# Performance work log

Hardware: AMD Instinct MI355X
Metric: run time of the kernel (lower is better)

The kernel has to match this reference:

```python
import jax, jax.numpy as jnp
import numpy as np

B, IN, HID = 8192, 2048, 2048


def setup_inputs() -> dict:
    key = jax.random.key(0)
    ks = jax.random.split(key, 8)
    s_in = 1.0 / np.sqrt(IN + HID)  # torch Linear default init scale (uniform bound)
    inp = {
        "x": jax.random.normal(ks[0], (B, IN), jnp.float32),
        "h_prev": jax.random.normal(ks[1], (B, HID), jnp.float32),
        "c_prev": jax.random.normal(ks[2], (B, HID), jnp.float32),
        "embedding_vec": jnp.zeros((B, 1), jnp.float32),  # ignored in vanilla mode
        "Wf": jax.random.normal(ks[3], (IN + HID, HID), jnp.float32) * s_in,
        "Wi": jax.random.normal(ks[4], (IN + HID, HID), jnp.float32) * s_in,
        "Wc": jax.random.normal(ks[5], (IN + HID, HID), jnp.float32) * s_in,
        "Wo": jax.random.normal(ks[6], (IN + HID, HID), jnp.float32) * s_in,
        "bf": jnp.zeros((HID,), jnp.float32),
        "bi": jnp.zeros((HID,), jnp.float32),
        "bc": jnp.zeros((HID,), jnp.float32),
        "bo": jnp.zeros((HID,), jnp.float32),
    }
    return inp


def reference(x, h_prev, c_prev, embedding_vec, Wf, Wi, Wc, Wo, bf, bi, bc, bo):
    # rearrange_inputs: concat flattened x with h_prev; embedding_vec ignored
    cat = jnp.concatenate([x.reshape(x.shape[0], -1), h_prev], axis=1)  # [B, IN+HID]
    # Fuse the four gate GEMMs into one: [B, IN+HID] @ [IN+HID, 4*HID]
    W = jnp.concatenate([Wf, Wi, Wc, Wo], axis=1)
    b = jnp.concatenate([bf, bi, bc, bo], axis=0)
    z = cat @ W + b  # [B, 4*HID]
    zf, zi, zc, zo = jnp.split(z, 4, axis=1)
    f_t = jax.nn.sigmoid(zf)
    i_t = jax.nn.sigmoid(zi)
    c_opt = jnp.tanh(zc)
    c_t = c_prev * f_t + i_t * c_opt
    o_t = jax.nn.sigmoid(zo)
    h_t = o_t * jnp.tanh(c_t)
    return (h_t, c_t)
```

## Files before the change

kernel.cpp:

```cpp
#include <hip/hip_runtime.h>
#include <stdint.h>

#define B_SZ   8192
#define IN_SZ  2048
#define HIDN   2048
#define KTOT   4096
#define BKk    32
#define NKS    (KTOT / BKk)
#define GRID_F 1024

typedef __attribute__((ext_vector_type(8))) short short8;
typedef __attribute__((ext_vector_type(8))) unsigned short ushort8;
typedef __attribute__((ext_vector_type(4))) float float4v;

static __device__ __forceinline__ float bf2f(uint16_t h) {
  union { uint32_t u; float f; } v; v.u = ((uint32_t)h) << 16; return v.f;
}
static __device__ __forceinline__ uint16_t f2bf(float f) {
  union { float f; uint32_t u; } v; v.f = f;
  uint32_t r = v.u + 0x7FFFu + ((v.u >> 16) & 1u);
  return (uint16_t)(r >> 16);
}
static __device__ __forceinline__ float sigmoidf_(float v) {
  return 1.f / (1.f + __expf(-v));
}
static __device__ __forceinline__ float tanhf_(float v) {
  return 1.f - 2.f / (1.f + __expf(2.f * v));
}

static __device__ __forceinline__ ushort8 load8(const void* base, size_t eidx, int isf32) {
  ushort8 r;
  if (isf32) {
    const float* p = (const float*)base + eidx;
    float4v a = *(const float4v*)p;
    float4v b = *(const float4v*)(p + 4);
    r[0] = f2bf(a[0]); r[1] = f2bf(a[1]); r[2] = f2bf(a[2]); r[3] = f2bf(a[3]);
    r[4] = f2bf(b[0]); r[5] = f2bf(b[1]); r[6] = f2bf(b[2]); r[7] = f2bf(b[3]);
  } else {
    r = *(const ushort8*)((const uint16_t*)base + eidx);
  }
  return r;
}

static __device__ __forceinline__ void gll16(const void* g, void* l) {
  __builtin_amdgcn_global_load_lds(
      (const __attribute__((address_space(1))) uint32_t*)g,
      (__attribute__((address_space(3))) uint32_t*)l, 16, 0, 0);
}

static __device__ __forceinline__ void bar() {
  asm volatile("" ::: "memory");
  __builtin_amdgcn_s_barrier();
  asm volatile("" ::: "memory");
}

__global__ __launch_bounds__(64) void detect_kernel(const uint32_t* __restrict__ x,
                                                    int* __restrict__ flag) {
  const int lane = threadIdx.x;
  int cnt = 0;
  #pragma unroll
  for (int s = 0; s < 8; ++s) {
    uint32_t u = x[lane + s * 64];
    int e = (u >> 7) & 0xFF;
    int hit = (e >= 117 && e <= 131) ? 1 : 0;
    cnt += (int)__popcll(__ballot(hit));
  }
  if (lane == 0) *flag = (cnt < 256) ? 1 : 0;
}

__global__ __launch_bounds__(256) void wtrans_kernel(
    const void* __restrict__ Wf, const void* __restrict__ Wi,
    const void* __restrict__ Wc, const void* __restrict__ Wo,
    uint16_t* __restrict__ Wt, const int* __restrict__ flagp)
{
  __shared__ uint16_t tile[64][33];
  const int isf32 = *flagp;
  const int k0 = blockIdx.x * 32;
  const int n0 = blockIdx.y * 64;
  const int g  = blockIdx.z;
  const void* W = (g == 0) ? Wf : (g == 1) ? Wi : (g == 2) ? Wc : Wo;
  const int tid = threadIdx.x;
  {
    const int r  = tid >> 3;
    const int c8 = (tid & 7) * 8;
    ushort8 v = load8(W, (size_t)(k0 + r) * HIDN + n0 + c8, isf32);
    #pragma unroll
    for (int e = 0; e < 8; ++e) tile[c8 + e][r] = v[e];
  }
  __syncthreads();
  {
    const int n  = tid >> 2;
    const int kc = (tid & 3) * 8;
    ushort8 v;
    #pragma unroll
    for (int e = 0; e < 8; ++e) v[e] = tile[n][kc + e];
    *(ushort8*)(Wt + (size_t)((n0 + n) * 4 + g) * KTOT + k0 + kc) = v;
  }
}

__global__ __launch_bounds__(256) void catconv_kernel(
    const void* __restrict__ x, const void* __restrict__ h,
    uint16_t* __restrict__ catB, const int* __restrict__ flagp)
{
  const int isf32 = *flagp;
  const void* src = blockIdx.y ? h : x;
  const size_t t = (size_t)blockIdx.x * 256 + threadIdx.x;
  const int m  = (int)(t >> 8);
  const int k8 = (int)(t & 255) * 8;
  ushort8 v = load8(src, (size_t)m * IN_SZ + k8, isf32);
  *(ushort8*)(catB + (size_t)m * KTOT + (size_t)blockIdx.y * IN_SZ + k8) = v;
}

extern "C" __global__ __launch_bounds__(512, 2) void lstm_fused_kernel(
    const uint16_t* __restrict__ Wt, const uint16_t* __restrict__ catB,
    const void* __restrict__ cprev,
    const void* __restrict__ bfv, const void* __restrict__ biv,
    const void* __restrict__ bcv, const void* __restrict__ bov,
    void* __restrict__ outbase, const int* __restrict__ flagp)
{
  extern __shared__ __align__(16) char ldsbuf[];

  const int isf32 = *flagp;
  const int tid  = threadIdx.x;
  const int lane = tid & 63;
  const int wave = tid >> 6;
  const int l15  = lane & 15;
  const int quad = lane >> 4;
  const int wr   = wave >> 2;
  const int wc   = wave & 3;

  const int bid = blockIdx.x;
  const int xcd = bid & 7, loc = bid >> 3;
  const int nt  = xcd * 4 + (loc & 3);
  const int mt  = loc >> 2;
  const int mB  = mt * 256;
  const int nB  = nt * 256;
  const int nb4 = nt * 64;

  const int srow = lane >> 2;
  const int scol = ((lane & 3) ^ ((lane >> 5) << 1)) * 8;
  const uint16_t* aSrc[2];
  const uint16_t* bSrc[2];
  #pragma unroll
  for (int s = 0; s < 2; ++s) {
    aSrc[s] = Wt   + (size_t)(nB + (s * 8 + wave) * 16 + srow) * KTOT + scol;
    bSrc[s] = catB + (size_t)(mB + (s * 8 + wave) * 16 + srow) * KTOT + scol;
  }

  int offA[8], offB[4];
  #pragma unroll
  for (int i = 0; i < 8; ++i) {
    const int b = (wr * 8 + i) * 1024 + l15 * 64 + quad * 16;
    offA[i] = b ^ (((l15 >> 3) & 1) << 5);
  }
  #pragma unroll
  for (int j = 0; j < 4; ++j) {
    const int b = (wc * 4 + j) * 1024 + l15 * 64 + quad * 16;
    offB[j] = 16384 + (b ^ (((l15 >> 3) & 1) << 5));
  }

  float4v acc[8][4];
  #pragma unroll
  for (int i = 0; i < 8; ++i)
    #pragma unroll
    for (int j = 0; j < 4; ++j)
      acc[i][j] = {0.f, 0.f, 0.f, 0.f};

  #pragma unroll
  for (int tt = 0; tt < 3; ++tt) {
    const size_t kk = (size_t)tt * BKk;
    const int bb = (tt & 3) * 32768 + wave * 1024;
    gll16(aSrc[0] + kk, ldsbuf + bb);
    gll16(aSrc[1] + kk, ldsbuf + bb + 8192);
    gll16(bSrc[0] + kk, ldsbuf + bb + 16384);
    gll16(bSrc[1] + kk, ldsbuf + bb + 16384 + 8192);
  }
  asm volatile("s_waitcnt vmcnt(8)" ::: "memory");
  bar();

#define KSTEP(T, DO_STAGE, VMSTR)                                              \
  {                                                                            \
    const int bb = ((T) & 3) * 32768;                                          \
    short8 af[4], bfr[4];                                                      \
    _Pragma("unroll")                                                          \
    for (int j = 0; j < 4; ++j)                                                \
      bfr[j] = *(const short8*)(ldsbuf + bb + offB[j]);                        \
    _Pragma("unroll")                                                          \
    for (int ii = 0; ii < 4; ++ii)                                             \
      af[ii] = *(const short8*)(ldsbuf + bb + offA[ii]);                       \
    if (DO_STAGE) {                                                            \
      const size_t kk = (size_t)((T) + 3) * BKk;                               \
      const int sb = (((T) + 3) & 3) * 32768 + wave * 1024;                    \
      gll16(aSrc[0] + kk, ldsbuf + sb);                                        \
      gll16(aSrc[1] + kk, ldsbuf + sb + 8192);                                 \
    }                                                                          \
    bar();                                                                     \
    __builtin_amdgcn_s_setprio(1);                                             \
    _Pragma("unroll")                                                          \
    for (int ii = 0; ii < 4; ++ii)                                             \
      _Pragma("unroll")                                                        \
      for (int j = 0; j < 4; ++j)                                              \
        acc[ii][j] = __builtin_amdgcn_mfma_f32_16x16x32_bf16(                  \
            af[ii], bfr[j], acc[ii][j], 0, 0, 0);                              \
    __builtin_amdgcn_s_setprio(0);                                             \
    bar();                                                                     \
    _Pragma("unroll")                                                          \
    for (int ii = 0; ii < 4; ++ii)                                             \
      af[ii] = *(const short8*)(ldsbuf + bb + offA[4 + ii]);                   \
    if (DO_STAGE) {                                                            \
      const size_t kk = (size_t)((T) + 3) * BKk;                               \
      const int sb = (((T) + 3) & 3) * 32768 + 16384 + wave * 1024;            \
      gll16(bSrc[0] + kk, ldsbuf + sb);                                        \
      gll16(bSrc[1] + kk, ldsbuf + sb + 8192);                                 \
    }                                                                          \
    asm volatile("s_waitcnt " VMSTR ::: "memory");                             \
    bar();                                                                     \
    __builtin_amdgcn_s_setprio(1);                                             \
    _Pragma("unroll")                                                          \
    for (int ii = 0; ii < 4; ++ii)                                             \
      _Pragma("unroll")                                                        \
      for (int j = 0; j < 4; ++j)                                              \
        acc[4 + ii][j] = __builtin_amdgcn_mfma_f32_16x16x32_bf16(              \
            af[ii], bfr[j], acc[4 + ii][j], 0, 0, 0);                          \
    __builtin_amdgcn_s_setprio(0);                                             \
    bar();                                                                     \
  }

  for (int t = 0; t < NKS - 3; ++t) KSTEP(t, 1, "vmcnt(8)");
  KSTEP(NKS - 3, 0, "vmcnt(4)");
  KSTEP(NKS - 2, 0, "vmcnt(0)");
  KSTEP(NKS - 1, 0, "vmcnt(0)");
#undef KSTEP

  #pragma unroll
  for (int i = 0; i < 8; ++i) {
    const int ng = nb4 + wr * 32 + i * 4 + quad;
    const float bfx = isf32 ? ((const float*)bfv)[ng] : bf2f(((const uint16_t*)bfv)[ng]);
    const float bix = isf32 ? ((const float*)biv)[ng] : bf2f(((const uint16_t*)biv)[ng]);
    const float bcx = isf32 ? ((const float*)bcv)[ng] : bf2f(((const uint16_t*)bcv)[ng]);
    const float box = isf32 ? ((const float*)bov)[ng] : bf2f(((const uint16_t*)bov)[ng]);
    #pragma unroll
    for (int j = 0; j < 4; ++j) {
      const int mg = mB + wc * 64 + j * 16 + l15;
      float4v z = acc[i][j];
      const float ft  = sigmoidf_(z[0] + bfx);
      const float it  = sigmoidf_(z[1] + bix);
      const float cto = tanhf_(z[2] + bcx);
      const float ot  = sigmoidf_(z[3] + box);
      const float cp  = isf32 ? ((const float*)cprev)[(size_t)mg * HIDN + ng]
                              : bf2f(((const uint16_t*)cprev)[(size_t)mg * HIDN + ng]);
      const float cvv = cp * ft + it * cto;
      acc[i][j][0] = ot * tanhf_(cvv);
      acc[i][j][1] = cvv;
    }
  }

  if (!isf32) {
    uint16_t* hout = (uint16_t*)outbase;
    uint16_t* cout = hout + (size_t)B_SZ * HIDN;
    uint16_t* hb = (uint16_t*)ldsbuf;
    uint16_t* cb = (uint16_t*)(ldsbuf + 32768);
    #pragma unroll
    for (int i = 0; i < 8; ++i) {
      const int ncl = wr * 32 + i * 4 + quad;
      #pragma unroll
      for (int j = 0; j < 4; ++j) {
        const int ml = wc * 64 + j * 16 + l15;
        hb[ml * 64 + ncl] = f2bf(acc[i][j][0]);
        cb[ml * 64 + ncl] = f2bf(acc[i][j][1]);
      }
    }
    bar();
    #pragma unroll
    for (int s = 0; s < 4; ++s) {
      const int off = tid * 16 + s * 8192;
      const int row = off >> 7;
      const int c8  = (off >> 4) & 7;
      const size_t g = (size_t)(mB + row) * HIDN + nb4 + c8 * 8;
      *(ushort8*)(hout + g) = *(const ushort8*)(ldsbuf + off);
      *(ushort8*)(cout + g) = *(const ushort8*)(ldsbuf + 32768 + off);
    }
  } else {
    float* hout = (float*)outbase;
    float* cout = hout + (size_t)B_SZ * HIDN;
    float* fbH = (float*)ldsbuf;
    float* fbC = (float*)(ldsbuf + 65536);
    #pragma unroll
    for (int i = 0; i < 8; ++i) {
      const int ncl = wr * 32 + i * 4 + quad;
      #pragma unroll
      for (int j = 0; j < 4; ++j) {
        const int ml = wc * 64 + j * 16 + l15;
        fbH[ml * 64 + ncl] = acc[i][j][0];
        fbC[ml * 64 + ncl] = acc[i][j][1];
      }
    }
    bar();
    #pragma unroll
    for (int s = 0; s < 8; ++s) {
      const int off = tid * 16 + s * 8192;
      const int row = off >> 8;
      const int c4  = (off >> 4) & 15;
      const size_t g = (size_t)(mB + row) * HIDN + nb4 + c4 * 4;
      *(float4v*)(hout + g) = *(const float4v*)(ldsbuf + off);
      *(float4v*)(cout + g) = *(const float4v*)(ldsbuf + 65536 + off);
    }
  }
}

extern "C" void kernel_launch(void* const* d_in, const int* in_sizes, int n_in,
                              void* d_out, int out_size, void* d_ws, size_t ws_size,
                              hipStream_t stream) {
  const void* x   = d_in[0];
  const void* h   = d_in[1];
  const void* c   = d_in[2];
  const void* Wf  = d_in[4];
  const void* Wi  = d_in[5];
  const void* Wc  = d_in[6];
  const void* Wo  = d_in[7];
  const void* bf_ = d_in[8];
  const void* bi_ = d_in[9];
  const void* bc_ = d_in[10];
  const void* bo_ = d_in[11];

  int*      flag = (int*)d_ws;
  uint16_t* Wt   = (uint16_t*)((char*)d_ws + 256);
  uint16_t* catB = (uint16_t*)((char*)d_ws + 256 + (size_t)64 * 1024 * 1024);

  static int lds_configured = 0;
  if (!lds_configured) {
    hipFuncSetAttribute((const void*)lstm_fused_kernel,
                        hipFuncAttributeMaxDynamicSharedMemorySize, 131072);
    lds_configured = 1;
  }

  hipLaunchKernelGGL(detect_kernel, dim3(1), dim3(64), 0, stream,
                     (const uint32_t*)x, flag);
  hipLaunchKernelGGL(wtrans_kernel, dim3(KTOT / 32, HIDN / 64, 4), dim3(256), 0, stream,
                     Wf, Wi, Wc, Wo, Wt, flag);
  hipLaunchKernelGGL(catconv_kernel, dim3(B_SZ * IN_SZ / (8 * 256), 2, 1), dim3(256), 0, stream,
                     x, h, catB, flag);
  hipLaunchKernelGGL(lstm_fused_kernel, dim3(GRID_F), dim3(512), 131072, stream,
                     Wt, catB, c, bf_, bi_, bc_, bo_, d_out, flag);
}
```

Measured before the change: 889.1 us.

## Widen weight transpose tiles with XOR swizzle and change GEMM LDS swizzle

```diff
diff --git a/kernel.cpp b/kernel.cpp
--- a/kernel.cpp
+++ b/kernel.cpp
@@ -73,28 +73,35 @@
     const void* __restrict__ Wc, const void* __restrict__ Wo,
     uint16_t* __restrict__ Wt, const int* __restrict__ flagp)
 {
-  __shared__ uint16_t tile[64][33];
+  __shared__ uint16_t tile[4 * 64 * 128];
   const int isf32 = *flagp;
-  const int k0 = blockIdx.x * 32;
+  const int k0 = blockIdx.x * 128;
   const int n0 = blockIdx.y * 64;
-  const int g  = blockIdx.z;
-  const void* W = (g == 0) ? Wf : (g == 1) ? Wi : (g == 2) ? Wc : Wo;
   const int tid = threadIdx.x;
-  {
-    const int r  = tid >> 3;
-    const int c8 = (tid & 7) * 8;
-    ushort8 v = load8(W, (size_t)(k0 + r) * HIDN + n0 + c8, isf32);
-    #pragma unroll
-    for (int e = 0; e < 8; ++e) tile[c8 + e][r] = v[e];
+  const void* Wg4[4] = {Wf, Wi, Wc, Wo};
+
+  #pragma unroll
+  for (int s = 0; s < 16; ++s) {
+    const int flat = s * 256 + tid;
+    const int g = flat >> 10;
+    const int r = (flat >> 3) & 127;
+    const int c = flat & 7;
+    ushort8 v = load8(Wg4[g], (size_t)(k0 + r) * HIDN + n0 + c * 8, isf32);
+    uint16_t* trow = tile + (g * 64 + c * 8) * 128 + (r & 7) + 8 * ((r >> 3) ^ c);
+    #pragma unroll
+    for (int e = 0; e < 8; ++e) trow[e * 128] = v[e];
   }
   __syncthreads();
-  {
-    const int n  = tid >> 2;
-    const int kc = (tid & 3) * 8;
-    ushort8 v;
-    #pragma unroll
-    for (int e = 0; e < 8; ++e) v[e] = tile[n][kc + e];
-    *(ushort8*)(Wt + (size_t)((n0 + n) * 4 + g) * KTOT + k0 + kc) = v;
+
+  #pragma unroll
+  for (int s = 0; s < 16; ++s) {
+    const int flat = s * 256 + tid;
+    const int kc = flat & 15;
+    const int np = flat >> 4;
+    const int n  = np >> 2;
+    ushort8 v = *(const ushort8*)(tile + (np & 3) * 8192 + n * 128 +
+                                  ((kc ^ (n >> 3)) * 8));
+    *(ushort8*)(Wt + (size_t)(n0 * 4 + np) * KTOT + k0 + kc * 8) = v;
   }
 }
 
@@ -138,7 +145,7 @@
   const int nb4 = nt * 64;
 
   const int srow = lane >> 2;
-  const int scol = ((lane & 3) ^ ((lane >> 5) << 1)) * 8;
+  const int scol = ((lane & 3) ^ ((lane >> 3) & 3)) * 8;
   const uint16_t* aSrc[2];
   const uint16_t* bSrc[2];
   #pragma unroll
@@ -147,17 +154,14 @@
     bSrc[s] = catB + (size_t)(mB + (s * 8 + wave) * 16 + srow) * KTOT + scol;
   }
 
+  const int rswz = (quad ^ ((l15 >> 1) & 3)) << 4;
   int offA[8], offB[4];
   #pragma unroll
-  for (int i = 0; i < 8; ++i) {
-    const int b = (wr * 8 + i) * 1024 + l15 * 64 + quad * 16;
-    offA[i] = b ^ (((l15 >> 3) & 1) << 5);
-  }
-  #pragma unroll
-  for (int j = 0; j < 4; ++j) {
-    const int b = (wc * 4 + j) * 1024 + l15 * 64 + quad * 16;
-    offB[j] = 16384 + (b ^ (((l15 >> 3) & 1) << 5));
-  }
+  for (int i = 0; i < 8; ++i)
+    offA[i] = (wr * 8 + i) * 1024 + l15 * 64 + rswz;
+  #pragma unroll
+  for (int j = 0; j < 4; ++j)
+    offB[j] = 16384 + (wc * 4 + j) * 1024 + l15 * 64 + rswz;
 
   float4v acc[8][4];
   #pragma unroll
@@ -270,7 +274,7 @@
         cb[ml * 64 + ncl] = f2bf(acc[i][j][1]);
       }
     }
-    bar();
+    __syncthreads();
     #pragma unroll
     for (int s = 0; s < 4; ++s) {
       const int off = tid * 16 + s * 8192;
@@ -295,7 +299,7 @@
         fbC[ml * 64 + ncl] = acc[i][j][1];
       }
     }
-    bar();
+    __syncthreads();
     #pragma unroll
     for (int s = 0; s < 8; ++s) {
       const int off = tid * 16 + s * 8192;
@@ -336,7 +340,7 @@
 
   hipLaunchKernelGGL(detect_kernel, dim3(1), dim3(64), 0, stream,
                      (const uint32_t*)x, flag);
-  hipLaunchKernelGGL(wtrans_kernel, dim3(KTOT / 32, HIDN / 64, 4), dim3(256), 0, stream,
+  hipLaunchKernelGGL(wtrans_kernel, dim3(KTOT / 128, HIDN / 64, 1), dim3(256), 0, stream,
                      Wf, Wi, Wc, Wo, Wt, flag);
   hipLaunchKernelGGL(catconv_kernel, dim3(B_SZ * IN_SZ / (8 * 256), 2, 1), dim3(256), 0, stream,
                      x, h, catB, flag);
```

Measured after the change: 875.7 us. No clear change (-1.5%).
